# Kernel optimization log

Hardware: AMD Instinct MI355X
Metric: run time of the kernel (lower is better)

The kernel has to match this reference:

```python
import jax, jax.numpy as jnp
import numpy as np

STEPS = 12
ALPHA = 0.1
LN_EPS = 1e-5
HEAD_DIM = 64


def setup_inputs() -> dict:
    key = jax.random.key(0)
    k0, k1, k2, k3 = jax.random.split(key, 4)
    B, N, D, H, Y, M = 8, 512, 768, 12, 64, 3072
    x = jax.random.normal(k0, (B, N, D), dtype=jnp.float32)
    Wq = jax.random.normal(k1, (H, Y, D), dtype=jnp.float32) * 0.02
    Wk = jax.random.normal(k2, (H, Y, D), dtype=jnp.float32) * 0.02
    xi = jax.random.normal(k3, (M, D), dtype=jnp.float32) * 0.02
    gamma = jnp.ones((D,), dtype=jnp.float32)
    delta = jnp.zeros((D,), dtype=jnp.float32)
    return {"x": x, "Wq": Wq, "Wk": Wk, "xi": xi, "gamma": gamma, "delta": delta}


def reference(x, Wq, Wk, xi, gamma, delta):
    beta = 1.0 / jnp.sqrt(jnp.asarray(HEAD_DIM, x.dtype))

    def layer_norm(t):
        mu = jnp.mean(t, axis=-1, keepdims=True)
        var = jnp.mean((t - mu) ** 2, axis=-1, keepdims=True)
        return gamma * (t - mu) * jax.lax.rsqrt(var + LN_EPS) + delta

    def energy(g):
        # g: [B, N, D]
        q = jnp.einsum("bnd,hyd->bhny", g, Wq)
        k = jnp.einsum("bmd,hyd->bhmy", g, Wk)
        scores = beta * jnp.einsum("bhny,bhmy->bhnm", q, k)  # [B,H,N,N]
        e_att = -(1.0 / beta) * jnp.sum(jax.nn.logsumexp(scores, axis=-1))
        hid = jnp.maximum(jnp.einsum("bnd,md->bnm", g, xi), 0.0)  # [B,N,M]
        e_hn = -0.5 * jnp.sum(hid * hid)
        return e_att + e_hn

    grad_e = jax.grad(energy)

    def step(xt, _):
        g = layer_norm(xt)          # gradient taken w.r.t. g, as in the paper
        xt = xt - ALPHA * grad_e(g)  # SGD update applied in x-space
        return xt, None

    x, _ = jax.lax.scan(step, x, None, length=STEPS)
    return x
```

## Files before the change

kernel.cpp:

```cpp
#include <hip/hip_runtime.h>

typedef _Float16 f16;
typedef __attribute__((ext_vector_type(8))) _Float16 half8;
typedef __attribute__((ext_vector_type(4))) _Float16 half4;
typedef __attribute__((ext_vector_type(4))) float f32x4;

#define Bb 8
#define Nn 512
#define Dd 768
#define Hh 12
#define Yy 64
#define Mm 3072
#define BN_TOT (Bb*Nn)
#define HY (Hh*Yy)
#define ALPHA 0.1f
#define BETA 0.125f
#define LN_EPS 1e-5f
#define SLICE ((size_t)BN_TOT * Dd)

__global__ __launch_bounds__(256) void k_ln(const float* __restrict__ x,
                                            const float* __restrict__ gamma,
                                            const float* __restrict__ delta,
                                            f16* __restrict__ g) {
  int row = blockIdx.x;
  const float* xr = x + (size_t)row * Dd;
  f16* gr = g + (size_t)row * Dd;
  int t = threadIdx.x;
  float v0 = xr[t], v1 = xr[t + 256], v2 = xr[t + 512];
  float s = v0 + v1 + v2;
  float ss = v0 * v0 + v1 * v1 + v2 * v2;
#pragma unroll
  for (int o = 32; o; o >>= 1) {
    s += __shfl_xor(s, o);
    ss += __shfl_xor(ss, o);
  }
  __shared__ float red[8];
  int wave = t >> 6;
  if ((t & 63) == 0) { red[wave] = s; red[4 + wave] = ss; }
  __syncthreads();
  float ts = red[0] + red[1] + red[2] + red[3];
  float tss = red[4] + red[5] + red[6] + red[7];
  float mu = ts * (1.0f / Dd);
  float var = tss * (1.0f / Dd) - mu * mu;
  float rstd = rsqrtf(var + LN_EPS);
  gr[t]       = (f16)(gamma[t]       * (v0 - mu) * rstd + delta[t]);
  gr[t + 256] = (f16)(gamma[t + 256] * (v1 - mu) * rstd + delta[t + 256]);
  gr[t + 512] = (f16)(gamma[t + 512] * (v2 - mu) * rstd + delta[t + 512]);
}

__global__ __launch_bounds__(256) void k_lnred(float* __restrict__ x,
                                               const float* __restrict__ gamma,
                                               const float* __restrict__ delta,
                                               f16* __restrict__ g,
                                               const f16* __restrict__ p03,
                                               const f16* __restrict__ p4,
                                               const f16* __restrict__ p5) {
  int row = blockIdx.x;
  float* xr = x + (size_t)row * Dd;
  f16* gr = g + (size_t)row * Dd;
  int t = threadIdx.x;
  float v[3];
#pragma unroll
  for (int e = 0; e < 3; ++e) {
    int c = t + e * 256;
    size_t off = (size_t)row * Dd + c;
    float add = (float)p03[off] + (float)p03[off + SLICE] + (float)p03[off + 2 * SLICE] +
                (float)p03[off + 3 * SLICE] + (float)p4[off] + (float)p5[off];
    v[e] = xr[c] + add;
    xr[c] = v[e];
  }
  float s = v[0] + v[1] + v[2];
  float ss = v[0] * v[0] + v[1] * v[1] + v[2] * v[2];
#pragma unroll
  for (int o = 32; o; o >>= 1) {
    s += __shfl_xor(s, o);
    ss += __shfl_xor(ss, o);
  }
  __shared__ float red[8];
  int wave = t >> 6;
  if ((t & 63) == 0) { red[wave] = s; red[4 + wave] = ss; }
  __syncthreads();
  float ts = red[0] + red[1] + red[2] + red[3];
  float tss = red[4] + red[5] + red[6] + red[7];
  float mu = ts * (1.0f / Dd);
  float var = tss * (1.0f / Dd) - mu * mu;
  float rstd = rsqrtf(var + LN_EPS);
#pragma unroll
  for (int e = 0; e < 3; ++e) {
    int c = t + e * 256;
    gr[c] = (f16)(gamma[c] * (v[e] - mu) * rstd + delta[c]);
  }
}

__global__ __launch_bounds__(256) void k_redfin(float* __restrict__ x,
                                                const f16* __restrict__ p03,
                                                const f16* __restrict__ p4,
                                                const f16* __restrict__ p5) {
  int row = blockIdx.x;
  float* xr = x + (size_t)row * Dd;
  int t = threadIdx.x;
#pragma unroll
  for (int e = 0; e < 3; ++e) {
    int c = t + e * 256;
    size_t off = (size_t)row * Dd + c;
    float add = (float)p03[off] + (float)p03[off + SLICE] + (float)p03[off + 2 * SLICE] +
                (float)p03[off + 3 * SLICE] + (float)p4[off] + (float)p5[off];
    xr[c] += add;
  }
}

__global__ __launch_bounds__(256) void k_cvt_tr(const float* __restrict__ in, int R, int C,
                                                f16* __restrict__ outB, f16* __restrict__ outT) {
  __shared__ float tile[64][65];
  int r0 = blockIdx.y * 64, c0 = blockIdx.x * 64;
  int tid = threadIdx.x;
#pragma unroll
  for (int e = 0; e < 16; ++e) {
    int idx = e * 256 + tid;
    int r = idx >> 6, c = idx & 63;
    float v = in[(size_t)(r0 + r) * C + c0 + c];
    tile[r][c] = v;
    outB[(size_t)(r0 + r) * C + c0 + c] = (f16)v;
  }
  __syncthreads();
#pragma unroll
  for (int e = 0; e < 16; ++e) {
    int idx = e * 256 + tid;
    int rr = idx >> 6, c = idx & 63;
    outT[(size_t)(c0 + rr) * R + r0 + c] = (f16)tile[c][rr];
  }
}

__device__ __forceinline__ void gl16(const f16* g, f16* l) {
  __builtin_amdgcn_global_load_lds(
      (const __attribute__((address_space(1))) void*)g,
      (__attribute__((address_space(3))) void*)l, 16, 0, 0);
}

template<int FM, int FN>
__device__ __forceinline__ void zacc(f32x4 (&a)[FM][FN]) {
  f32x4 z = {0.f, 0.f, 0.f, 0.f};
#pragma unroll
  for (int i = 0; i < FM; ++i)
#pragma unroll
    for (int j = 0; j < FN; ++j) a[i][j] = z;
}

template<int BM, int BN, int WM, int WN>
__device__ __forceinline__ void gemm_core(const f16* __restrict__ A, int lda, int row0,
                                          const f16* __restrict__ Bt, int ldb, int col0,
                                          int K,
                                          f32x4 (&acc)[BM / WM / 16][BN / WN / 16],
                                          f16* sA, f16* sB) {
  constexpr int FM = BM / WM / 16, FN = BN / WN / 16;
  const int tid = threadIdx.x;
  const int w = tid >> 6, lane = tid & 63;
  const int wm = (WN == 1) ? w : (w >> 1);
  const int wn = (WN == 1) ? 0 : (w & 1);
  const int m0 = wm * (BM / WM), n0 = wn * (BN / WN);
  const int lr = lane & 15, lk = lane >> 4;
  const int srow = lane >> 2;
  const int scol = (lane & 3) * 8;
  for (int k0 = 0; k0 < K; k0 += 32) {
#pragma unroll
    for (int t = 0; t < BM / 64; ++t) {
      int r0 = w * (BM / 4) + t * 16;
      gl16(A + (size_t)(row0 + r0 + srow) * lda + k0 + scol, sA + r0 * 32);
    }
#pragma unroll
    for (int t = 0; t < BN / 64; ++t) {
      int r0 = w * (BN / 4) + t * 16;
      gl16(Bt + (size_t)(col0 + r0 + srow) * ldb + k0 + scol, sB + r0 * 32);
    }
    __syncthreads();
    half8 af[FM], bfr[FN];
#pragma unroll
    for (int i = 0; i < FM; ++i)
      af[i] = *(const half8*)(sA + (m0 + i * 16 + lr) * 32 + lk * 8);
#pragma unroll
    for (int j = 0; j < FN; ++j)
      bfr[j] = *(const half8*)(sB + (n0 + j * 16 + lr) * 32 + lk * 8);
#pragma unroll
    for (int i = 0; i < FM; ++i)
#pragma unroll
      for (int j = 0; j < FN; ++j)
        acc[i][j] = __builtin_amdgcn_mfma_f32_16x16x32_f16(af[i], bfr[j], acc[i][j], 0, 0, 0);
    __syncthreads();
  }
}

__global__ __launch_bounds__(256) void k_qkproj(const f16* __restrict__ g,
                                                const f16* __restrict__ Wqh,
                                                const f16* __restrict__ Wkh,
                                                f16* __restrict__ q, f16* __restrict__ k,
                                                f16* __restrict__ qT, f16* __restrict__ kT) {
  __shared__ f16 sA[128 * 32], sB[128 * 32];
  int lin = blockIdx.x + blockIdx.y * 6 + blockIdx.z * 192;
  int swz = (lin & 7) * 48 + (lin >> 3);
  int col0 = (swz % 6) * 128;
  int row0 = ((swz / 6) & 31) * 128;
  int zq = swz / 192;
  const f16* Wh = zq ? Wkh : Wqh;
  f16* out = zq ? k : q;
  f16* outT = zq ? kT : qT;
  f32x4 acc[4][4];
  zacc(acc);
  gemm_core<128, 128, 2, 2>(g, Dd, row0, Wh, Dd, col0, Dd, acc, sA, sB);
  int w = threadIdx.x >> 6, lane = threadIdx.x & 63;
  int m0 = (w >> 1) * 64, n0 = (w & 1) * 64, lr = lane & 15, lk = lane >> 4;
#pragma unroll
  for (int i = 0; i < 4; ++i)
#pragma unroll
    for (int j = 0; j < 4; ++j) {
      int r0g = row0 + m0 + i * 16 + lk * 4;
      int cg = col0 + n0 + j * 16 + lr;
      half4 hv;
#pragma unroll
      for (int p = 0; p < 4; ++p) {
        f16 h1 = (f16)acc[i][j][p];
        out[(size_t)(r0g + p) * HY + cg] = h1;
        hv[p] = h1;
      }
      int b = r0g >> 9, nl = r0g & 511;
      int h = cg >> 6, y = cg & 63;
      *(half4*)(outT + (((size_t)b * Hh + h) * Yy + y) * Nn + nl) = hv;
    }
}

__global__ __launch_bounds__(256) void k_scores(const f16* __restrict__ q,
                                                const f16* __restrict__ k,
                                                f16* __restrict__ SP, int zbase) {
  __shared__ f16 sA[128 * 32], sB[128 * 32];
  int zg = zbase + blockIdx.z;
  int b = zg / Hh, h = zg - b * Hh;
  const f16* A = q + (size_t)b * Nn * HY + h * Yy;
  const f16* Bt = k + (size_t)b * Nn * HY + h * Yy;
  int row0 = blockIdx.y * 128, col0 = blockIdx.x * 128;
  f32x4 acc[4][4];
  zacc(acc);
  gemm_core<128, 128, 2, 2>(A, HY, row0, Bt, HY, col0, Yy, acc, sA, sB);
  f16* S = SP + (size_t)blockIdx.z * Nn * Nn;
  int w = threadIdx.x >> 6, lane = threadIdx.x & 63;
  int m0 = (w >> 1) * 64, n0 = (w & 1) * 64, lr = lane & 15, lk = lane >> 4;
#pragma unroll
  for (int i = 0; i < 4; ++i)
#pragma unroll
    for (int j = 0; j < 4; ++j) {
      int r0g = row0 + m0 + i * 16 + lk * 4;
      int cg = col0 + n0 + j * 16 + lr;
#pragma unroll
      for (int p = 0; p < 4; ++p)
        S[(size_t)(r0g + p) * Nn + cg] = (f16)(BETA * acc[i][j][p]);
    }
}

__global__ __launch_bounds__(256) void k_softmax(f16* __restrict__ SP) {
  f16* row = SP + ((size_t)blockIdx.y * Nn + blockIdx.x) * Nn;
  int t = threadIdx.x;
  float a = (float)row[t], b = (float)row[t + 256];
  float mx = fmaxf(a, b);
#pragma unroll
  for (int o = 32; o; o >>= 1) mx = fmaxf(mx, __shfl_xor(mx, o));
  __shared__ float rm[4], rs[4];
  int wave = t >> 6;
  if ((t & 63) == 0) rm[wave] = mx;
  __syncthreads();
  mx = fmaxf(fmaxf(rm[0], rm[1]), fmaxf(rm[2], rm[3]));
  float ea = __expf(a - mx), eb = __expf(b - mx);
  float s = ea + eb;
#pragma unroll
  for (int o = 32; o; o >>= 1) s += __shfl_xor(s, o);
  if ((t & 63) == 0) rs[wave] = s;
  __syncthreads();
  float inv = 1.0f / (rs[0] + rs[1] + rs[2] + rs[3]);
  row[t] = (f16)(ea * inv);
  row[t + 256] = (f16)(eb * inv);
}

__global__ __launch_bounds__(256) void k_transP(const f16* __restrict__ SP, f16* __restrict__ PT) {
  __shared__ f16 tile[64][72];
  const f16* P = SP + (size_t)blockIdx.z * Nn * Nn;
  f16* T = PT + (size_t)blockIdx.z * Nn * Nn;
  int nb = blockIdx.y * 64, mb = blockIdx.x * 64;
  int tid = threadIdx.x;
#pragma unroll
  for (int e = 0; e < 2; ++e) {
    int ci = e * 256 + tid;
    int r = ci >> 3, c = (ci & 7) * 8;
    half8 v = *(const half8*)(P + (size_t)(nb + r) * Nn + mb + c);
#pragma unroll
    for (int qq = 0; qq < 8; ++qq) tile[r][c + qq] = v[qq];
  }
  __syncthreads();
#pragma unroll
  for (int e = 0; e < 2; ++e) {
    int ci = e * 256 + tid;
    int r = ci >> 3, c = (ci & 7) * 8;
    half8 v;
#pragma unroll
    for (int qq = 0; qq < 8; ++qq) v[qq] = tile[c + qq][r];
    *(half8*)(T + (size_t)(mb + r) * Nn + nb + c) = v;
  }
}

__global__ __launch_bounds__(256) void k_dqdk(const f16* __restrict__ SP,
                                              const f16* __restrict__ PT,
                                              const f16* __restrict__ qT,
                                              const f16* __restrict__ kT,
                                              f16* __restrict__ dq,
                                              f16* __restrict__ dk, int zbase) {
  __shared__ f16 sA[128 * 32], sB[64 * 32];
  int which = blockIdx.z & 1, zloc = blockIdx.z >> 1;
  int zg = zbase + zloc;
  int b = zg / Hh, h = zg - b * Hh;
  const f16* A = (which ? PT : SP) + (size_t)zloc * Nn * Nn;
  const f16* Bt = (which ? qT : kT) + (size_t)zg * Yy * Nn;
  f16* out = which ? dk : dq;
  int row0 = blockIdx.y * 128;
  f32x4 acc[2][4];
  zacc(acc);
  gemm_core<128, 64, 4, 1>(A, Nn, row0, Bt, Nn, 0, Nn, acc, sA, sB);
  int w = threadIdx.x >> 6, lane = threadIdx.x & 63;
  int m0 = w * 32, lr = lane & 15, lk = lane >> 4;
#pragma unroll
  for (int i = 0; i < 2; ++i)
#pragma unroll
    for (int j = 0; j < 4; ++j) {
      int r0g = row0 + m0 + i * 16 + lk * 4;
      int cg = j * 16 + lr;
#pragma unroll
      for (int p = 0; p < 4; ++p)
        out[(size_t)(b * Nn + r0g + p) * HY + h * Yy + cg] = (f16)acc[i][j][p];
    }
}

__global__ __launch_bounds__(256) void k_update(const f16* __restrict__ dq,
                                                const f16* __restrict__ dk,
                                                const f16* __restrict__ WqT,
                                                const f16* __restrict__ WkT,
                                                const f16* __restrict__ hid,
                                                const f16* __restrict__ xiT,
                                                f16* __restrict__ p03,
                                                f16* __restrict__ p4,
                                                f16* __restrict__ p5) {
  __shared__ f16 sA[128 * 32], sB[128 * 32];
  int lin = blockIdx.x + blockIdx.y * 6 + blockIdx.z * 192;
  int swz = (lin & 7) * 144 + (lin >> 3);
  int col0 = (swz % 6) * 128;
  int row0 = ((swz / 6) & 31) * 128;
  int zz = swz / 192;
  const f16* A; const f16* Bt; int lda, ldb;
  if (zz == 0)      { A = dq; Bt = WqT; lda = HY; ldb = HY; }
  else if (zz == 1) { A = dk; Bt = WkT; lda = HY; ldb = HY; }
  else              { A = hid + (zz - 2) * 768; Bt = xiT + (zz - 2) * 768; lda = Mm; ldb = Mm; }
  f16* outp = (zz == 0) ? p4 : (zz == 1) ? p5 : p03 + (size_t)(zz - 2) * SLICE;
  f32x4 acc[4][4];
  zacc(acc);
  gemm_core<128, 128, 2, 2>(A, lda, row0, Bt, ldb, col0, 768, acc, sA, sB);
  int w = threadIdx.x >> 6, lane = threadIdx.x & 63;
  int m0 = (w >> 1) * 64, n0 = (w & 1) * 64, lr = lane & 15, lk = lane >> 4;
#pragma unroll
  for (int i = 0; i < 4; ++i)
#pragma unroll
    for (int j = 0; j < 4; ++j) {
      int r0g = row0 + m0 + i * 16 + lk * 4;
      int cg = col0 + n0 + j * 16 + lr;
#pragma unroll
      for (int p = 0; p < 4; ++p)
        outp[(size_t)(r0g + p) * Dd + cg] = (f16)(ALPHA * acc[i][j][p]);
    }
}

__global__ __launch_bounds__(256) void k_hid(const f16* __restrict__ g, const f16* __restrict__ xih,
                                             f16* __restrict__ hid) {
  __shared__ f16 sA[128 * 32], sB[128 * 32];
  int lin = blockIdx.x + blockIdx.y * 24;
  int swz = (lin & 7) * 96 + (lin >> 3);
  int col0 = (swz % 24) * 128;
  int row0 = (swz / 24) * 128;
  f32x4 acc[4][4];
  zacc(acc);
  gemm_core<128, 128, 2, 2>(g, Dd, row0, xih, Dd, col0, Dd, acc, sA, sB);
  int w = threadIdx.x >> 6, lane = threadIdx.x & 63;
  int m0 = (w >> 1) * 64, n0 = (w & 1) * 64, lr = lane & 15, lk = lane >> 4;
#pragma unroll
  for (int i = 0; i < 4; ++i)
#pragma unroll
    for (int j = 0; j < 4; ++j) {
      int r0g = row0 + m0 + i * 16 + lk * 4;
      int cg = col0 + n0 + j * 16 + lr;
#pragma unroll
      for (int p = 0; p < 4; ++p)
        hid[(size_t)(r0g + p) * Mm + cg] = (f16)fmaxf(acc[i][j][p], 0.0f);
    }
}

extern "C" void kernel_launch(void* const* d_in, const int* in_sizes, int n_in,
                              void* d_out, int out_size, void* d_ws, size_t ws_size,
                              hipStream_t stream) {
  const float* x_in  = (const float*)d_in[0];
  const float* Wq    = (const float*)d_in[1];
  const float* Wk    = (const float*)d_in[2];
  const float* xi    = (const float*)d_in[3];
  const float* gamma = (const float*)d_in[4];
  const float* delta = (const float*)d_in[5];
  float* x = (float*)d_out;

  char* p = (char*)d_ws;
  size_t used = 0;
  auto alloc = [&](size_t elems) -> f16* {
    size_t bytes = (elems * sizeof(f16) + 255) & ~(size_t)255;
    f16* r = (f16*)(p + used);
    used += bytes;
    return r;
  };
  const size_t SZ = (size_t)BN_TOT * HY;
  f16* g   = alloc(SZ);
  f16* q   = alloc(SZ);
  f16* k   = alloc(SZ);
  f16* qT  = alloc(SZ);
  f16* kT  = alloc(SZ);
  f16* dq  = alloc(SZ);
  f16* dk  = alloc(SZ);
  f16* Wqh = alloc((size_t)HY * Dd);
  f16* Wkh = alloc((size_t)HY * Dd);
  f16* WqT = alloc((size_t)Dd * HY);
  f16* WkT = alloc((size_t)Dd * HY);
  f16* xih = alloc((size_t)Mm * Dd);
  f16* xiT = alloc((size_t)Dd * Mm);
  f16* SP  = alloc((size_t)48 * Nn * Nn);
  f16* PTH = alloc((size_t)48 * Nn * Nn);
  f16* hid = PTH;
  if (used > ws_size) return;

  hipMemcpyAsync(x, x_in, SZ * sizeof(float), hipMemcpyDeviceToDevice, stream);

  k_cvt_tr<<<dim3(Dd / 64, HY / 64), 256, 0, stream>>>(Wq, HY, Dd, Wqh, WqT);
  k_cvt_tr<<<dim3(Dd / 64, HY / 64), 256, 0, stream>>>(Wk, HY, Dd, Wkh, WkT);
  k_cvt_tr<<<dim3(Dd / 64, Mm / 64), 256, 0, stream>>>(xi, Mm, Dd, xih, xiT);

  for (int step = 0; step < 12; ++step) {
    if (step == 0)
      k_ln<<<BN_TOT, 256, 0, stream>>>(x, gamma, delta, g);
    else
      k_lnred<<<BN_TOT, 256, 0, stream>>>(x, gamma, delta, g, SP, q, k);
    k_qkproj<<<dim3(6, 32, 2), 256, 0, stream>>>(g, Wqh, Wkh, q, k, qT, kT);
    for (int half = 0; half < 2; ++half) {
      int zbase = half * 48;
      k_scores<<<dim3(Nn / 128, Nn / 128, 48), 256, 0, stream>>>(q, k, SP, zbase);
      k_softmax<<<dim3(Nn, 48), 256, 0, stream>>>(SP);
      k_transP<<<dim3(8, 8, 48), 256, 0, stream>>>(SP, PTH);
      k_dqdk<<<dim3(1, Nn / 128, 96), 256, 0, stream>>>(SP, PTH, qT, kT, dq, dk, zbase);
    }
    k_hid<<<dim3(24, 32), 256, 0, stream>>>(g, xih, hid);
    k_update<<<dim3(6, 32, 6), 256, 0, stream>>>(dq, dk, WqT, WkT, hid, xiT, SP, q, k);
  }
  k_redfin<<<BN_TOT, 256, 0, stream>>>(x, SP, q, k);
}
```

Measured before the change: 2.671 ms.

## Fuse score GEMM, softmax and probability transpose into one attention kernel

Replaces the separate scores GEMM, row softmax and transpose kernels with a single kernel. Each block computes a full 32x512 row strip of scores, does the max and sum reductions in registers and shared memory, and writes both P and its transpose directly. This removes two extra round trips of the 48x512x512 half-precision score tensor through global memory, plus two kernel launches. In exchange the key tile is much larger in shared memory, the transposed writes are strided half4 stores, and there is less reuse per block in the small GEMM.

```diff
diff --git a/kernel.cpp b/kernel.cpp
--- a/kernel.cpp
+++ b/kernel.cpp
@@ -227,80 +227,125 @@
     }
 }
 
-__global__ __launch_bounds__(256) void k_scores(const f16* __restrict__ q,
-                                                const f16* __restrict__ k,
-                                                f16* __restrict__ SP, int zbase) {
-  __shared__ f16 sA[128 * 32], sB[128 * 32];
-  int zg = zbase + blockIdx.z;
+__global__ __launch_bounds__(256) void k_attn(const f16* __restrict__ q,
+                                              const f16* __restrict__ k,
+                                              f16* __restrict__ SP,
+                                              f16* __restrict__ PT, int zbase) {
+  __shared__ f16 sA[32 * 32], sB[512 * 32];
+  __shared__ float redm[4][32], redl[4][32];
+  int zloc = blockIdx.y;
+  int zg = zbase + zloc;
   int b = zg / Hh, h = zg - b * Hh;
   const f16* A = q + (size_t)b * Nn * HY + h * Yy;
   const f16* Bt = k + (size_t)b * Nn * HY + h * Yy;
-  int row0 = blockIdx.y * 128, col0 = blockIdx.x * 128;
-  f32x4 acc[4][4];
+  int r0 = blockIdx.x * 32;
+  int tid = threadIdx.x, w = tid >> 6, lane = tid & 63;
+  int lr = lane & 15, lk = lane >> 4;
+  int srow = lane >> 2, scol = (lane & 3) * 8;
+  f32x4 acc[2][8];
   zacc(acc);
-  gemm_core<128, 128, 2, 2>(A, HY, row0, Bt, HY, col0, Yy, acc, sA, sB);
-  f16* S = SP + (size_t)blockIdx.z * Nn * Nn;
-  int w = threadIdx.x >> 6, lane = threadIdx.x & 63;
-  int m0 = (w >> 1) * 64, n0 = (w & 1) * 64, lr = lane & 15, lk = lane >> 4;
-#pragma unroll
-  for (int i = 0; i < 4; ++i)
-#pragma unroll
-    for (int j = 0; j < 4; ++j) {
-      int r0g = row0 + m0 + i * 16 + lk * 4;
-      int cg = col0 + n0 + j * 16 + lr;
-#pragma unroll
-      for (int p = 0; p < 4; ++p)
-        S[(size_t)(r0g + p) * Nn + cg] = (f16)(BETA * acc[i][j][p]);
-    }
-}
-
-__global__ __launch_bounds__(256) void k_softmax(f16* __restrict__ SP) {
-  f16* row = SP + ((size_t)blockIdx.y * Nn + blockIdx.x) * Nn;
-  int t = threadIdx.x;
-  float a = (float)row[t], b = (float)row[t + 256];
-  float mx = fmaxf(a, b);
-#pragma unroll
-  for (int o = 32; o; o >>= 1) mx = fmaxf(mx, __shfl_xor(mx, o));
-  __shared__ float rm[4], rs[4];
-  int wave = t >> 6;
-  if ((t & 63) == 0) rm[wave] = mx;
+  for (int k0 = 0; k0 < Yy; k0 += 32) {
+    if (w < 2)
+      gl16(A + (size_t)(r0 + w * 16 + srow) * HY + k0 + scol, sA + (w * 16) * 32);
+#pragma unroll
+    for (int t = 0; t < 8; ++t)
+      gl16(Bt + (size_t)(w * 128 + t * 16 + srow) * HY + k0 + scol, sB + (w * 128 + t * 16) * 32);
+    __syncthreads();
+    half8 af[2], bfr[8];
+#pragma unroll
+    for (int i = 0; i < 2; ++i)
+      af[i] = *(const half8*)(sA + (i * 16 + lr) * 32 + lk * 8);
+#pragma unroll
+    for (int j = 0; j < 8; ++j)
+      bfr[j] = *(const half8*)(sB + (w * 128 + j * 16 + lr) * 32 + lk * 8);
+#pragma unroll
+    for (int i = 0; i < 2; ++i)
+#pragma unroll
+      for (int j = 0; j < 8; ++j)
+        acc[i][j] = __builtin_amdgcn_mfma_f32_16x16x32_f16(af[i], bfr[j], acc[i][j], 0, 0, 0);
+    __syncthreads();
+  }
+  float pm[2][4];
+#pragma unroll
+  for (int i = 0; i < 2; ++i)
+#pragma unroll
+    for (int p = 0; p < 4; ++p) {
+      float m = -1e30f;
+#pragma unroll
+      for (int j = 0; j < 8; ++j) {
+        acc[i][j][p] *= BETA;
+        m = fmaxf(m, acc[i][j][p]);
+      }
+      pm[i][p] = m;
+    }
+#pragma unroll
+  for (int o = 1; o < 16; o <<= 1)
+#pragma unroll
+    for (int i = 0; i < 2; ++i)
+#pragma unroll
+      for (int p = 0; p < 4; ++p) pm[i][p] = fmaxf(pm[i][p], __shfl_xor(pm[i][p], o));
+  if (lr == 0)
+#pragma unroll
+    for (int i = 0; i < 2; ++i)
+#pragma unroll
+      for (int p = 0; p < 4; ++p) redm[w][i * 16 + lk * 4 + p] = pm[i][p];
   __syncthreads();
-  mx = fmaxf(fmaxf(rm[0], rm[1]), fmaxf(rm[2], rm[3]));
-  float ea = __expf(a - mx), eb = __expf(b - mx);
-  float s = ea + eb;
-#pragma unroll
-  for (int o = 32; o; o >>= 1) s += __shfl_xor(s, o);
-  if ((t & 63) == 0) rs[wave] = s;
+  float fm[2][4], ps[2][4];
+#pragma unroll
+  for (int i = 0; i < 2; ++i)
+#pragma unroll
+    for (int p = 0; p < 4; ++p) {
+      int r = i * 16 + lk * 4 + p;
+      fm[i][p] = fmaxf(fmaxf(redm[0][r], redm[1][r]), fmaxf(redm[2][r], redm[3][r]));
+      ps[i][p] = 0.f;
+    }
+#pragma unroll
+  for (int i = 0; i < 2; ++i)
+#pragma unroll
+    for (int j = 0; j < 8; ++j)
+#pragma unroll
+      for (int p = 0; p < 4; ++p) {
+        float e = __expf(acc[i][j][p] - fm[i][p]);
+        acc[i][j][p] = e;
+        ps[i][p] += e;
+      }
+#pragma unroll
+  for (int o = 1; o < 16; o <<= 1)
+#pragma unroll
+    for (int i = 0; i < 2; ++i)
+#pragma unroll
+      for (int p = 0; p < 4; ++p) ps[i][p] += __shfl_xor(ps[i][p], o);
+  if (lr == 0)
+#pragma unroll
+    for (int i = 0; i < 2; ++i)
+#pragma unroll
+      for (int p = 0; p < 4; ++p) redl[w][i * 16 + lk * 4 + p] = ps[i][p];
   __syncthreads();
-  float inv = 1.0f / (rs[0] + rs[1] + rs[2] + rs[3]);
-  row[t] = (f16)(ea * inv);
-  row[t + 256] = (f16)(eb * inv);
-}
-
-__global__ __launch_bounds__(256) void k_transP(const f16* __restrict__ SP, f16* __restrict__ PT) {
-  __shared__ f16 tile[64][72];
-  const f16* P = SP + (size_t)blockIdx.z * Nn * Nn;
-  f16* T = PT + (size_t)blockIdx.z * Nn * Nn;
-  int nb = blockIdx.y * 64, mb = blockIdx.x * 64;
-  int tid = threadIdx.x;
-#pragma unroll
-  for (int e = 0; e < 2; ++e) {
-    int ci = e * 256 + tid;
-    int r = ci >> 3, c = (ci & 7) * 8;
-    half8 v = *(const half8*)(P + (size_t)(nb + r) * Nn + mb + c);
-#pragma unroll
-    for (int qq = 0; qq < 8; ++qq) tile[r][c + qq] = v[qq];
-  }
-  __syncthreads();
-#pragma unroll
-  for (int e = 0; e < 2; ++e) {
-    int ci = e * 256 + tid;
-    int r = ci >> 3, c = (ci & 7) * 8;
-    half8 v;
-#pragma unroll
-    for (int qq = 0; qq < 8; ++qq) v[qq] = tile[c + qq][r];
-    *(half8*)(T + (size_t)(mb + r) * Nn + nb + c) = v;
-  }
+  float inv[2][4];
+#pragma unroll
+  for (int i = 0; i < 2; ++i)
+#pragma unroll
+    for (int p = 0; p < 4; ++p) {
+      int r = i * 16 + lk * 4 + p;
+      inv[i][p] = 1.0f / (redl[0][r] + redl[1][r] + redl[2][r] + redl[3][r]);
+    }
+  f16* S = SP + (size_t)zloc * Nn * Nn;
+  f16* T = PT + (size_t)zloc * Nn * Nn;
+#pragma unroll
+  for (int i = 0; i < 2; ++i)
+#pragma unroll
+    for (int j = 0; j < 8; ++j) {
+      int row = r0 + i * 16 + lk * 4;
+      int col = w * 128 + j * 16 + lr;
+      half4 hv;
+#pragma unroll
+      for (int p = 0; p < 4; ++p) {
+        f16 v = (f16)(acc[i][j][p] * inv[i][p]);
+        S[(size_t)(row + p) * Nn + col] = v;
+        hv[p] = v;
+      }
+      *(half4*)(T + (size_t)col * Nn + row) = hv;
+    }
 }
 
 __global__ __launch_bounds__(256) void k_dqdk(const f16* __restrict__ SP,
@@ -447,9 +492,7 @@
     k_qkproj<<<dim3(6, 32, 2), 256, 0, stream>>>(g, Wqh, Wkh, q, k, qT, kT);
     for (int half = 0; half < 2; ++half) {
       int zbase = half * 48;
-      k_scores<<<dim3(Nn / 128, Nn / 128, 48), 256, 0, stream>>>(q, k, SP, zbase);
-      k_softmax<<<dim3(Nn, 48), 256, 0, stream>>>(SP);
-      k_transP<<<dim3(8, 8, 48), 256, 0, stream>>>(SP, PTH);
+      k_attn<<<dim3(16, 48), 256, 0, stream>>>(q, k, SP, PTH, zbase);
       k_dqdk<<<dim3(1, Nn / 128, 96), 256, 0, stream>>>(SP, PTH, qT, kT, dq, dk, zbase);
     }
     k_hid<<<dim3(24, 32), 256, 0, stream>>>(g, xih, hid);
```

New measurement: 2.245 ms. -16.0%, faster.
